# Optimization experiments

Measured on AMD Instinct MI355X. Metric: run time of the kernel, lower is better.

Reference implementation:

```python
import jax, jax.numpy as jnp
import numpy as np

B, N, QD, H, D = 2, 2048, 1152, 16, 72
INNER = H * D
RETAIN_RATE = 0.4  # layer_count in [4, 64] branch
N_KEEP = int(N * RETAIN_RATE)
N_PRUNE = N - N_KEEP
SCALE = D ** (-0.5)


def setup_inputs() -> dict:
    key = jax.random.key(0)
    ks = jax.random.split(key, 6)
    s = 0.02
    return {
        "x": jax.random.normal(ks[0], (B, N, QD), jnp.float32),
        "Wq": jax.random.normal(ks[1], (QD, INNER), jnp.float32) * s,
        "Wk": jax.random.normal(ks[2], (QD, INNER), jnp.float32) * s,
        "Wv": jax.random.normal(ks[3], (QD, INNER), jnp.float32) * s,
        "Wo": jax.random.normal(ks[4], (INNER, QD), jnp.float32) * s,
        "bo": jnp.zeros((QD,), jnp.float32),
    }


def reference(x, Wq, Wk, Wv, Wo, bo):
    b = x.shape[0]
    # self-attention: context = x
    q = (x @ Wq).reshape(b, N, H, D).transpose(0, 2, 1, 3)  # [b,H,N,D]
    k = (x @ Wk).reshape(b, N, H, D).transpose(0, 2, 1, 3)
    v = (x @ Wv).reshape(b, N, H, D).transpose(0, 2, 1, 3)

    # ---- WPR pruning pass: full attention map, mean over heads ----
    logits = jnp.einsum('bhnd,bhmd->bhnm', q, k) * SCALE  # [b,H,N,N]
    M = jax.nn.softmax(logits, axis=-1)
    attn = M.mean(axis=1)  # [b,N,N]

    # 5-step power iteration: dist = (1/N) @ attn^5
    dist = jnp.full((b, 1, N), 1.0 / N, dtype=attn.dtype)
    for _ in range(5):
        dist = dist @ attn
    importance = dist[:, 0]  # [b,N]

    _, imp_inds = jax.lax.top_k(importance, N_KEEP)
    _, prune_inds = jax.lax.top_k(-importance, N_PRUNE)
    # boolean-mask selection in torch returns rows in ascending index order
    sorted_imp = jnp.sort(imp_inds, axis=1)      # [b,N_KEEP]
    sorted_prune = jnp.sort(prune_inds, axis=1)  # [b,N_PRUNE]

    selected_rows = jnp.take_along_axis(attn, sorted_imp[:, :, None], axis=1)  # [b,N_KEEP,N]
    max_inds = jnp.argmax(selected_rows, axis=1)  # [b,N]: most-attending retained row per token
    sim_inds = jnp.take_along_axis(max_inds, sorted_prune, axis=1)  # [b,N_PRUNE]

    # ---- attention among retained tokens only ----
    gi = sorted_imp[:, None, :, None]  # broadcast gather index
    q_r = jnp.take_along_axis(q, gi, axis=2)  # [b,H,N_KEEP,D]
    k_r = jnp.take_along_axis(k, gi, axis=2)
    v_r = jnp.take_along_axis(v, gi, axis=2)
    attn_r = jax.nn.softmax(jnp.einsum('bhnd,bhmd->bhnm', q_r, k_r) * SCALE, axis=-1)
    out_r = jnp.einsum('bhnm,bhmd->bhnd', attn_r, v_r)  # [b,H,N_KEEP,D]
    out_r = out_r.transpose(0, 2, 1, 3).reshape(b, N_KEEP, INNER)

    # similarity-based recovery for pruned tokens
    out_p = jnp.take_along_axis(out_r, sim_inds[:, :, None], axis=1)  # [b,N_PRUNE,INNER]

    bidx = jnp.arange(b)[:, None]
    out = jnp.zeros((b, N, INNER), out_r.dtype)
    out = out.at[bidx, sorted_imp].set(out_r)
    out = out.at[bidx, sorted_prune].set(out_p)

    return out @ Wo + bo
```

## Files before the change

kernel.cpp:

```cpp
#include <hip/hip_runtime.h>

namespace {
constexpr int B = 2;
constexpr int N = 2048;
constexpr int QD = 1152;
constexpr int H = 16;
constexpr int D = 72;
constexpr int INNER = 1152;
constexpr int NKEEP = 819;
constexpr int PSL = 32;
constexpr int ILEN = N / PSL;
constexpr int DP = 80;
constexpr int LSTR = 88;
constexpr int ASL = 16;
constexpr int ACH = (NKEEP + ASL - 1) / ASL;
constexpr int ROWS = B * H * N;
constexpr int X4 = (B * N * QD) / 4;
}

#define FINF __builtin_inff()
#define SCALE 0.11785113019775793f

typedef __attribute__((ext_vector_type(8))) __bf16 bf16x8;
typedef __attribute__((ext_vector_type(16))) float f32x16;
typedef __attribute__((ext_vector_type(8))) short short8;
typedef __attribute__((ext_vector_type(4))) short short4v;

__device__ __forceinline__ f32x16 mfma_bf16(bf16x8 a, bf16x8 b, f32x16 c) {
  return __builtin_amdgcn_mfma_f32_32x32x16_bf16(a, b, c, 0, 0, 0);
}
__device__ __forceinline__ short f2bf(float x) {
  unsigned u = __float_as_uint(x);
  unsigned r = (u + 0x7fffu + ((u >> 16) & 1u)) >> 16;
  return (short)r;
}
__device__ __forceinline__ float bf2f(short b) {
  return __uint_as_float(((unsigned)(unsigned short)b) << 16);
}

__global__ __launch_bounds__(256) void k_prep(
    const float* __restrict__ X, short* __restrict__ Xh, short* __restrict__ Xl,
    short* __restrict__ qkv)
{
  int g = blockIdx.x * 256 + threadIdx.x;
  if (g < X4) {
    float4 v = ((const float4*)X)[g];
    float vv[4] = {v.x, v.y, v.z, v.w};
    short4v h, l;
#pragma unroll
    for (int i = 0; i < 4; ++i) {
      short hb = f2bf(vv[i]);
      h[i] = hb;
      l[i] = f2bf(vv[i] - bf2f(hb));
    }
    *(short4v*)(void*)(Xh + (size_t)g * 4) = h;
    *(short4v*)(void*)(Xl + (size_t)g * 4) = l;
  } else {
    int t = g - X4;
    int arr = t / ROWS, row = t - arr * ROWS;
    *(float4*)(void*)(qkv + (size_t)arr * ROWS * DP + (size_t)row * DP + 72) =
        make_float4(0.f, 0.f, 0.f, 0.f);
  }
}

__global__ __launch_bounds__(256) void k_wsplit4(
    const float* __restrict__ W0, const float* __restrict__ W1,
    const float* __restrict__ W2, const float* __restrict__ W3,
    short* __restrict__ WTh, short* __restrict__ WTl,
    short* __restrict__ WoTh, short* __restrict__ WoTl)
{
  __shared__ float tile[64][65];
  const int tid = threadIdx.x;
  const int k0 = blockIdx.y * 64, n0 = blockIdx.x * 64;
  const int z = blockIdx.z;
  const float* W = (z == 0) ? W0 : (z == 1) ? W1 : (z == 2) ? W2 : W3;
  short* outH = (z < 3) ? WTh + (size_t)z * QD * INNER : WoTh;
  short* outL = (z < 3) ? WTl + (size_t)z * QD * INNER : WoTl;
  {
    int r = tid >> 2, c0 = (tid & 3) * 16;
#pragma unroll
    for (int j = 0; j < 16; j += 4) {
      float4 v = *(const float4*)&W[(size_t)(k0 + r) * 1152 + n0 + c0 + j];
      tile[r][c0 + j] = v.x; tile[r][c0 + j + 1] = v.y;
      tile[r][c0 + j + 2] = v.z; tile[r][c0 + j + 3] = v.w;
    }
  }
  __syncthreads();
  for (int e = tid; e < 4096; e += 256) {
    int nr = e >> 6, kc = e & 63;
    float v = tile[kc][nr];
    short hb = f2bf(v);
    outH[(size_t)(n0 + nr) * 1152 + k0 + kc] = hb;
    outL[(size_t)(n0 + nr) * 1152 + k0 + kc] = f2bf(v - bf2f(hb));
  }
}

__global__ __launch_bounds__(256, 2) void k_pgemm3(
    const short* __restrict__ Ah_g, const short* __restrict__ Al_g,
    const short* __restrict__ Bh_g, const short* __restrict__ Bl_g,
    short* __restrict__ QKV0)
{
  constexpr int LK = 40;
  __shared__ short AhS[128 * LK], AlS[128 * LK], BhS[128 * LK], BlS[128 * LK];
  const int tid = threadIdx.x;
  const int wv = tid >> 6, ln = tid & 63;
  const int col = ln & 31, hi = ln >> 5;
  const int wm = wv >> 1, wn = wv & 1;
  const int swz = (blockIdx.x & 7) * 108 + (blockIdx.x >> 3);
  const int m0 = (swz / 27) * 128, n0 = (swz % 27) * 128;

  f32x16 acc[2][2];
#pragma unroll
  for (int mi = 0; mi < 2; ++mi)
#pragma unroll
    for (int ni = 0; ni < 2; ++ni)
#pragma unroll
      for (int r = 0; r < 16; ++r) acc[mi][ni][r] = 0.f;

  for (int kt = 0; kt < 1152; kt += 32) {
    __syncthreads();
    for (int e = tid; e < 512; e += 256) {
      int r = e >> 2, c4 = e & 3;
      size_t sa = (size_t)(m0 + r) * 1152 + kt + c4 * 8;
      *(float4*)&AhS[r * LK + c4 * 8] = *(const float4*)(Ah_g + sa);
      *(float4*)&AlS[r * LK + c4 * 8] = *(const float4*)(Al_g + sa);
      size_t sb = (size_t)(n0 + r) * 1152 + kt + c4 * 8;
      *(float4*)&BhS[r * LK + c4 * 8] = *(const float4*)(Bh_g + sb);
      *(float4*)&BlS[r * LK + c4 * 8] = *(const float4*)(Bl_g + sb);
    }
    __syncthreads();
#pragma unroll
    for (int kc = 0; kc < 2; ++kc) {
      bf16x8 ah[2], al[2], bh[2], bl[2];
#pragma unroll
      for (int mi = 0; mi < 2; ++mi) {
        int r = wm * 64 + mi * 32 + col;
        ah[mi] = *(const bf16x8*)&AhS[r * LK + kc * 16 + hi * 8];
        al[mi] = *(const bf16x8*)&AlS[r * LK + kc * 16 + hi * 8];
      }
#pragma unroll
      for (int ni = 0; ni < 2; ++ni) {
        int r = wn * 64 + ni * 32 + col;
        bh[ni] = *(const bf16x8*)&BhS[r * LK + kc * 16 + hi * 8];
        bl[ni] = *(const bf16x8*)&BlS[r * LK + kc * 16 + hi * 8];
      }
#pragma unroll
      for (int mi = 0; mi < 2; ++mi)
#pragma unroll
        for (int ni = 0; ni < 2; ++ni) {
          acc[mi][ni] = mfma_bf16(ah[mi], bh[ni], acc[mi][ni]);
          acc[mi][ni] = mfma_bf16(ah[mi], bl[ni], acc[mi][ni]);
          acc[mi][ni] = mfma_bf16(al[mi], bh[ni], acc[mi][ni]);
        }
    }
  }
  const size_t S = (size_t)65536 * 80;
#pragma unroll
  for (int mi = 0; mi < 2; ++mi)
#pragma unroll
    for (int ni = 0; ni < 2; ++ni)
#pragma unroll
      for (int r = 0; r < 16; ++r) {
        int m = m0 + wm * 64 + mi * 32 + (r & 3) + 8 * (r >> 2) + 4 * hi;
        int c = n0 + wn * 64 + ni * 32 + col;
        int which = c / 1152, cm = c - which * 1152;
        int hh = cm / 72, dd = cm - hh * 72;
        int b = m >> 11, nn = m & 2047;
        size_t idx = (((size_t)(b * 16 + hh)) * 2048 + nn) * 80 + dd;
        float v = acc[mi][ni][r];
        short hb = f2bf(v);
        short* OH = QKV0 + (size_t)which * 2 * S;
        OH[idx] = hb;
        OH[S + idx] = f2bf(v - bf2f(hb));
      }
}

__global__ __launch_bounds__(256, 2) void k_stats3(
    const short* __restrict__ Qh, const short* __restrict__ Ql,
    const short* __restrict__ Kh, const short* __restrict__ Kl,
    float* __restrict__ ssum)
{
  __shared__ __align__(16) short kh[64 * LSTR];
  __shared__ __align__(16) short kl[64 * LSTR];
  const int tid = threadIdx.x;
  const int wv = tid >> 6, ln = tid & 63;
  const int col = ln & 31, hi = ln >> 5;
  const int hb = blockIdx.x & 31;
  const int rest = blockIdx.x >> 5;
  const int q0 = (rest & 7) * 256;
  const int ks = rest >> 3;
  const int h = hb >> 1, b = hb & 1;
  const size_t bhbase = (size_t)(b * H + h) * N * DP;
  const int kbeg = ks * (N / 2), kend = kbeg + N / 2;

  bf16x8 qfh[2][5], qfl[2][5];
#pragma unroll
  for (int mi = 0; mi < 2; ++mi) {
    const size_t rb = bhbase + (size_t)(q0 + wv * 64 + mi * 32 + col) * DP + hi * 8;
#pragma unroll
    for (int d = 0; d < 5; ++d) {
      qfh[mi][d] = *(const bf16x8*)(const void*)(Qh + rb + d * 16);
      qfl[mi][d] = *(const bf16x8*)(const void*)(Ql + rb + d * 16);
    }
  }
  float s[2][16];
#pragma unroll
  for (int mi = 0; mi < 2; ++mi)
#pragma unroll
    for (int r = 0; r < 16; ++r) s[mi][r] = 0.f;

  float4 rkh[3], rkl[3];
  auto LOADK = [&](int kt) {
#pragma unroll
    for (int ss = 0; ss < 3; ++ss) {
      int e = ss * 256 + tid;
      if (e < 640) {
        int r = e / 10, cc = e - r * 10;
        size_t sb = bhbase + (size_t)(kt + r) * DP + cc * 8;
        rkh[ss] = *(const float4*)(const void*)(Kh + sb);
        rkl[ss] = *(const float4*)(const void*)(Kl + sb);
      }
    }
  };
  auto STOREK = [&]() {
#pragma unroll
    for (int ss = 0; ss < 3; ++ss) {
      int e = ss * 256 + tid;
      if (e < 640) {
        int r = e / 10, cc = e - r * 10;
        *(float4*)(void*)(kh + r * LSTR + cc * 8) = rkh[ss];
        *(float4*)(void*)(kl + r * LSTR + cc * 8) = rkl[ss];
      }
    }
  };

  LOADK(kbeg);
  for (int kt = kbeg; kt < kend; kt += 64) {
    __syncthreads();
    STOREK();
    __syncthreads();
    if (kt + 64 < kend) LOADK(kt + 64);
    f32x16 z[2][2];
#pragma unroll
    for (int mi = 0; mi < 2; ++mi)
#pragma unroll
      for (int rn = 0; rn < 2; ++rn)
#pragma unroll
        for (int r = 0; r < 16; ++r) z[mi][rn][r] = 0.f;
#pragma unroll
    for (int d = 0; d < 5; ++d) {
      const int boff = d * 16 + hi * 8;
      bf16x8 bh0 = *(const bf16x8*)(const void*)(kh + col * LSTR + boff);
      bf16x8 bl0 = *(const bf16x8*)(const void*)(kl + col * LSTR + boff);
      bf16x8 bh1 = *(const bf16x8*)(const void*)(kh + (32 + col) * LSTR + boff);
      bf16x8 bl1 = *(const bf16x8*)(const void*)(kl + (32 + col) * LSTR + boff);
#pragma unroll
      for (int mi = 0; mi < 2; ++mi) {
        z[mi][0] = mfma_bf16(qfh[mi][d], bh0, z[mi][0]);
        z[mi][0] = mfma_bf16(qfh[mi][d], bl0, z[mi][0]);
        z[mi][0] = mfma_bf16(qfl[mi][d], bh0, z[mi][0]);
        z[mi][1] = mfma_bf16(qfh[mi][d], bh1, z[mi][1]);
        z[mi][1] = mfma_bf16(qfh[mi][d], bl1, z[mi][1]);
        z[mi][1] = mfma_bf16(qfl[mi][d], bh1, z[mi][1]);
      }
    }
#pragma unroll
    for (int mi = 0; mi < 2; ++mi)
#pragma unroll
      for (int r = 0; r < 16; ++r)
        s[mi][r] += __expf(z[mi][0][r] * SCALE) + __expf(z[mi][1][r] * SCALE);
  }
#pragma unroll
  for (int mi = 0; mi < 2; ++mi)
#pragma unroll
    for (int r = 0; r < 16; ++r) {
      float v = s[mi][r];
#pragma unroll
      for (int o = 1; o < 32; o <<= 1) v += __shfl_xor(v, o);
      if (col == 0) {
        int row = q0 + wv * 64 + mi * 32 + ((r & 3) + ((r >> 2) << 3) + (hi << 2));
        ssum[(size_t)ks * ROWS + (size_t)(b * H + h) * N + row] = v;
      }
    }
}

__global__ __launch_bounds__(256) void k_sinv(
    const float* __restrict__ ssum, float* __restrict__ inv_out)
{
  int g = blockIdx.x * 256 + threadIdx.x;
  if (g < ROWS) inv_out[g] = 1.0f / (ssum[g] + ssum[(size_t)ROWS + g]);
}

__global__ __launch_bounds__(256, 2) void k_attn3(
    const short* __restrict__ Qh, const short* __restrict__ Ql,
    const short* __restrict__ Kh, const short* __restrict__ Kl,
    const float* __restrict__ inv_in, float* __restrict__ attn,
    float* __restrict__ part8)
{
  __shared__ __align__(16) short kh[64 * LSTR];
  __shared__ __align__(16) short kl[64 * LSTR];
  __shared__ float invs[256];
  __shared__ float colred[64][8];
  const int tid = threadIdx.x;
  const int wv = tid >> 6, ln = tid & 63;
  const int col = ln & 31, hi = ln >> 5;
  const int q0 = (blockIdx.x & 7) * 256;
  const int b = (blockIdx.x >> 3) & 1;
  const int k0 = (blockIdx.x >> 4) * 64;

  f32x16 pa[2][2];
#pragma unroll
  for (int mi = 0; mi < 2; ++mi)
#pragma unroll
    for (int rn = 0; rn < 2; ++rn)
#pragma unroll
      for (int r = 0; r < 16; ++r) pa[mi][rn][r] = 0.f;

  float4 rkh[3], rkl[3];
  float rin;
  auto LOADH = [&](int h) {
    const size_t hb = (size_t)(b * H + h) * N * DP;
#pragma unroll
    for (int ss = 0; ss < 3; ++ss) {
      int e = ss * 256 + tid;
      if (e < 640) {
        int r = e / 10, cc = e - r * 10;
        size_t sb = hb + (size_t)(k0 + r) * DP + cc * 8;
        rkh[ss] = *(const float4*)(const void*)(Kh + sb);
        rkl[ss] = *(const float4*)(const void*)(Kl + sb);
      }
    }
    rin = inv_in[(size_t)(b * H + h) * N + q0 + tid];
  };
  auto STOREH = [&]() {
#pragma unroll
    for (int ss = 0; ss < 3; ++ss) {
      int e = ss * 256 + tid;
      if (e < 640) {
        int r = e / 10, cc = e - r * 10;
        *(float4*)(void*)(kh + r * LSTR + cc * 8) = rkh[ss];
        *(float4*)(void*)(kl + r * LSTR + cc * 8) = rkl[ss];
      }
    }
    invs[tid] = rin;
  };

  LOADH(0);
  for (int h = 0; h < H; ++h) {
    __syncthreads();
    STOREH();
    __syncthreads();
    if (h + 1 < H) LOADH(h + 1);

    const size_t bhbase = (size_t)(b * H + h) * N * DP;
    f32x16 z[2][2];
#pragma unroll
    for (int mi = 0; mi < 2; ++mi)
#pragma unroll
      for (int rn = 0; rn < 2; ++rn)
#pragma unroll
        for (int r = 0; r < 16; ++r) z[mi][rn][r] = 0.f;

#pragma unroll
    for (int d = 0; d < 5; ++d) {
      const int boff = d * 16 + hi * 8;
      bf16x8 bh0 = *(const bf16x8*)(const void*)(kh + col * LSTR + boff);
      bf16x8 bl0 = *(const bf16x8*)(const void*)(kl + col * LSTR + boff);
      bf16x8 bh1 = *(const bf16x8*)(const void*)(kh + (32 + col) * LSTR + boff);
      bf16x8 bl1 = *(const bf16x8*)(const void*)(kl + (32 + col) * LSTR + boff);
      bf16x8 qh0 = *(const bf16x8*)(const void*)(Qh + bhbase + (size_t)(q0 + wv * 64 + col) * DP + boff);
      bf16x8 ql0 = *(const bf16x8*)(const void*)(Ql + bhbase + (size_t)(q0 + wv * 64 + col) * DP + boff);
      bf16x8 qh1 = *(const bf16x8*)(const void*)(Qh + bhbase + (size_t)(q0 + wv * 64 + 32 + col) * DP + boff);
      bf16x8 ql1 = *(const bf16x8*)(const void*)(Ql + bhbase + (size_t)(q0 + wv * 64 + 32 + col) * DP + boff);
      z[0][0] = mfma_bf16(qh0, bh0, z[0][0]);
      z[0][0] = mfma_bf16(qh0, bl0, z[0][0]);
      z[0][0] = mfma_bf16(ql0, bh0, z[0][0]);
      z[0][1] = mfma_bf16(qh0, bh1, z[0][1]);
      z[0][1] = mfma_bf16(qh0, bl1, z[0][1]);
      z[0][1] = mfma_bf16(ql0, bh1, z[0][1]);
      z[1][0] = mfma_bf16(qh1, bh0, z[1][0]);
      z[1][0] = mfma_bf16(qh1, bl0, z[1][0]);
      z[1][0] = mfma_bf16(ql1, bh0, z[1][0]);
      z[1][1] = mfma_bf16(qh1, bh1, z[1][1]);
      z[1][1] = mfma_bf16(qh1, bl1, z[1][1]);
      z[1][1] = mfma_bf16(ql1, bh1, z[1][1]);
    }
#pragma unroll
    for (int mi = 0; mi < 2; ++mi)
#pragma unroll
      for (int r = 0; r < 16; ++r) {
        const int rloc = wv * 64 + mi * 32 + (r & 3) + ((r >> 2) << 3) + (hi << 2);
        const float iv = invs[rloc];
        pa[mi][0][r] += __expf(z[mi][0][r] * SCALE) * iv;
        pa[mi][1][r] += __expf(z[mi][1][r] * SCALE) * iv;
      }
  }
  const float invH = 1.0f / H;
#pragma unroll
  for (int mi = 0; mi < 2; ++mi)
#pragma unroll
    for (int r = 0; r < 16; ++r) {
      const int row = q0 + wv * 64 + mi * 32 + (r & 3) + ((r >> 2) << 3) + (hi << 2);
      attn[((size_t)b * N + row) * N + k0 + col] = pa[mi][0][r] * invH;
      attn[((size_t)b * N + row) * N + k0 + 32 + col] = pa[mi][1][r] * invH;
    }
  __syncthreads();
#pragma unroll
  for (int rn = 0; rn < 2; ++rn) {
    float s = 0.f;
#pragma unroll
    for (int mi = 0; mi < 2; ++mi)
#pragma unroll
      for (int r = 0; r < 16; ++r) s += pa[mi][rn][r];
    colred[rn * 32 + col][wv * 2 + hi] = s * invH;
  }
  __syncthreads();
  if (tid < 64) {
    float s = 0.f;
#pragma unroll
    for (int u = 0; u < 8; ++u) s += colred[tid][u];
    part8[(size_t)(q0 >> 8) * (B * N) + b * N + k0 + tid] = s * (1.0f / N);
  }
}

__global__ __launch_bounds__(256) void k_powfused(
    const float* __restrict__ attn, const float* __restrict__ partial_in,
    float* __restrict__ partial_out, int nin)
{
  __shared__ float red[4][64];
  __shared__ float ds[64];
  const int tid = threadIdx.x;
  const int g = blockIdx.x * 256 + tid;
  const int sy = blockIdx.y;
  const int b = g / N, j = g % N;
  const int i0 = sy * ILEN;
  {
    int i = tid & 63, sgrp = tid >> 6;
    const int per = nin >> 2;
    const float* p = partial_in + (size_t)(b * N + i0 + i);
    float s8 = 0.f;
    for (int k = 0; k < per; ++k) s8 += p[(size_t)(sgrp * per + k) * (B * N)];
    red[sgrp][i] = s8;
  }
  __syncthreads();
  if (tid < 64) ds[tid] = red[0][tid] + red[1][tid] + red[2][tid] + red[3][tid];
  __syncthreads();
  const float* ab = attn + (size_t)b * N * N;
  float s0 = 0.f, s1 = 0.f, s2 = 0.f, s3 = 0.f;
  for (int i = 0; i < ILEN; i += 4) {
    s0 += ds[i + 0] * ab[(size_t)(i0 + i + 0) * N + j];
    s1 += ds[i + 1] * ab[(size_t)(i0 + i + 1) * N + j];
    s2 += ds[i + 2] * ab[(size_t)(i0 + i + 2) * N + j];
    s3 += ds[i + 3] * ab[(size_t)(i0 + i + 3) * N + j];
  }
  partial_out[(size_t)sy * (B * N) + g] = (s0 + s1) + (s2 + s3);
}

__global__ __launch_bounds__(1024) void k_partition(
    const float* __restrict__ partial, int* __restrict__ sorted_imp,
    int* __restrict__ keepflag, int* __restrict__ s_map)
{
  __shared__ float v[N];
  __shared__ int   id[N];
  __shared__ int   kf[N];
  __shared__ int   ps[N];
  const int tid = threadIdx.x;
  const int b = blockIdx.x;
  for (int i = tid; i < N; i += 1024) {
    float s = 0.f;
    const float* p = partial + (size_t)(b * N + i);
    for (int sy = 0; sy < PSL; ++sy) s += p[(size_t)sy * (B * N)];
    v[i] = s; id[i] = i;
  }
  for (int k = 2; k <= N; k <<= 1) {
    for (int j = k >> 1; j > 0; j >>= 1) {
      __syncthreads();
      for (int i = tid; i < N; i += 1024) {
        int ixj = i ^ j;
        if (ixj > i) {
          bool up = ((i & k) == 0);
          float va = v[i], vb = v[ixj];
          int ia = id[i], ib = id[ixj];
          bool b_before_a = (vb > va) || (vb == va && ib < ia);
          if (b_before_a == up) { v[i] = vb; v[ixj] = va; id[i] = ib; id[ixj] = ia; }
        }
      }
    }
  }
  __syncthreads();
  for (int i = tid; i < N; i += 1024) kf[id[i]] = (i < NKEEP) ? 1 : 0;
  __syncthreads();
  for (int i = tid; i < N; i += 1024) ps[i] = kf[i];
  for (int off = 1; off < N; off <<= 1) {
    __syncthreads();
    int t0 = (tid >= off) ? ps[tid - off] : 0;
    int i1 = tid + 1024;
    int t1 = ps[i1 - off];
    __syncthreads();
    ps[tid] += t0;
    ps[i1] += t1;
  }
  __syncthreads();
  for (int i = tid; i < N; i += 1024) {
    int excl = ps[i] - kf[i];
    keepflag[b * N + i] = kf[i];
    if (kf[i]) { sorted_imp[b * NKEEP + excl] = i; s_map[b * N + i] = excl; }
  }
}

__global__ __launch_bounds__(256) void k_argmax_part(
    const float* __restrict__ attn, const int* __restrict__ sorted_imp,
    float* __restrict__ pval, int* __restrict__ pidx)
{
  __shared__ int imp_s[ACH];
  const int tid = threadIdx.x;
  const int g = blockIdx.x * 256 + tid;
  const int s = blockIdx.y;
  const int b = g / N, n = g % N;
  const int k0 = s * ACH;
  const int k1 = (k0 + ACH < NKEEP) ? k0 + ACH : NKEEP;
  const int cnt = k1 - k0;
  for (int i = tid; i < cnt; i += 256) imp_s[i] = sorted_imp[b * NKEEP + k0 + i];
  __syncthreads();
  const float* ab = attn + (size_t)b * N * N;
  float best = -FINF; int bi = k0;
  for (int k = 0; k < cnt; ++k) {
    float val = ab[(size_t)imp_s[k] * N + n];
    if (val > best) { best = val; bi = k0 + k; }
  }
  pval[(size_t)s * (B * N) + g] = best;
  pidx[(size_t)s * (B * N) + g] = bi;
}

__global__ __launch_bounds__(256) void k_argmax_comb(
    const float* __restrict__ pval, const int* __restrict__ pidx,
    const int* __restrict__ keepflag, int* __restrict__ s_map)
{
  int g = blockIdx.x * 256 + threadIdx.x;
  if (g >= B * N) return;
  float best = -FINF; int bi = 0;
#pragma unroll
  for (int s = 0; s < ASL; ++s) {
    float v = pval[(size_t)s * (B * N) + g];
    if (v > best) { best = v; bi = pidx[(size_t)s * (B * N) + g]; }
  }
  if (!keepflag[g]) s_map[g] = bi;
}

__global__ __launch_bounds__(256, 2) void k_rfused(
    const short* __restrict__ Qh, const short* __restrict__ Ql,
    const short* __restrict__ Kh, const short* __restrict__ Kl,
    const short* __restrict__ Vh, const int* __restrict__ sorted_imp,
    short* __restrict__ Yh, short* __restrict__ Yl)
{
  constexpr int LK = 88;
  constexpr int VTS = 72;
  __shared__ __align__(16) short KhS[64 * LK];
  __shared__ __align__(16) short KlS[64 * LK];
  __shared__ __align__(16) short VhS[64 * LK];
  __shared__ __align__(16) short VT[72 * VTS];
  __shared__ int imp[NKEEP];
  const int tid = threadIdx.x;
  const int wv = tid >> 6, ln = tid & 63;
  const int col = ln & 31, hi = ln >> 5;
  const int b = blockIdx.z, h = blockIdx.y, q0 = blockIdx.x * 128;
  const size_t bh80 = (size_t)(b * H + h) * N * DP;
  for (int i = tid; i < NKEEP; i += 256) imp[i] = sorted_imp[b * NKEEP + i];
  __syncthreads();
  int qr = q0 + wv * 32 + col;
  int qi = imp[qr < NKEEP ? qr : NKEEP - 1];
  bf16x8 qfh[5], qfl[5];
  {
    const size_t qb = bh80 + (size_t)qi * DP + hi * 8;
#pragma unroll
    for (int d = 0; d < 5; ++d) {
      qfh[d] = *(const bf16x8*)(const void*)(Qh + qb + d * 16);
      qfl[d] = *(const bf16x8*)(const void*)(Ql + qb + d * 16);
    }
  }
  float denom = 0.f;
  f32x16 oacc[3];
#pragma unroll
  for (int nc = 0; nc < 3; ++nc)
#pragma unroll
    for (int r = 0; r < 16; ++r) oacc[nc][r] = 0.f;

  for (int kt = 0; kt < 832; kt += 64) {
    for (int e = tid; e < 640; e += 256) {
      int r = e / 10, cc = e - r * 10;
      int kv = kt + r;
      float4 vkh, vkl, vvh;
      if (kv < NKEEP) {
        size_t sb = bh80 + (size_t)imp[kv] * DP + cc * 8;
        vkh = *(const float4*)(const void*)(Kh + sb);
        vkl = *(const float4*)(const void*)(Kl + sb);
        vvh = *(const float4*)(const void*)(Vh + sb);
      } else {
        vkh = make_float4(0.f, 0.f, 0.f, 0.f); vkl = vkh; vvh = vkh;
      }
      *(float4*)(void*)&KhS[r * LK + cc * 8] = vkh;
      *(float4*)(void*)&KlS[r * LK + cc * 8] = vkl;
      *(float4*)(void*)&VhS[r * LK + cc * 8] = vvh;
    }
    __syncthreads();
    f32x16 z[2];
#pragma unroll
    for (int rn = 0; rn < 2; ++rn)
#pragma unroll
      for (int r = 0; r < 16; ++r) z[rn][r] = 0.f;
#pragma unroll
    for (int d = 0; d < 5; ++d) {
      const int boff = d * 16 + hi * 8;
#pragma unroll
      for (int rn = 0; rn < 2; ++rn) {
        bf16x8 kfh = *(const bf16x8*)(const void*)(KhS + (rn * 32 + col) * LK + boff);
        bf16x8 kfl = *(const bf16x8*)(const void*)(KlS + (rn * 32 + col) * LK + boff);
        z[rn] = mfma_bf16(kfh, qfh[d], z[rn]);
        z[rn] = mfma_bf16(kfh, qfl[d], z[rn]);
        z[rn] = mfma_bf16(kfl, qfh[d], z[rn]);
      }
    }
    for (int e = tid; e < 576; e += 256) {
      int dd = e % 72, k8 = e / 72;
      short8 t;
#pragma unroll
      for (int j = 0; j < 8; ++j) t[j] = VhS[(k8 * 8 + j) * LK + dd];
      *(short8*)(void*)&VT[dd * VTS + k8 * 8] = t;
    }
    const bool full = (kt + 64 <= NKEEP);
#pragma unroll
    for (int rn = 0; rn < 2; ++rn) {
      int kvb = kt + rn * 32 + 4 * hi;
#pragma unroll
      for (int r = 0; r < 16; ++r) {
        float pe = __expf(z[rn][r] * SCALE);
        if (!full) {
          int kv = kvb + (r & 3) + 8 * (r >> 2);
          pe = (kv < NKEEP) ? pe : 0.f;
        }
        z[rn][r] = pe;
        denom += pe;
      }
    }
    __syncthreads();
#pragma unroll
    for (int rn = 0; rn < 2; ++rn) {
#pragma unroll
      for (int kc = 0; kc < 2; ++kc) {
        unsigned p0, p1, p2, p3;
        asm("v_cvt_pk_bf16_f32 %0, %1, %2" : "=v"(p0) : "v"(z[rn][8 * kc + 0]), "v"(z[rn][8 * kc + 1]));
        asm("v_cvt_pk_bf16_f32 %0, %1, %2" : "=v"(p1) : "v"(z[rn][8 * kc + 2]), "v"(z[rn][8 * kc + 3]));
        asm("v_cvt_pk_bf16_f32 %0, %1, %2" : "=v"(p2) : "v"(z[rn][8 * kc + 4]), "v"(z[rn][8 * kc + 5]));
        asm("v_cvt_pk_bf16_f32 %0, %1, %2" : "=v"(p3) : "v"(z[rn][8 * kc + 6]), "v"(z[rn][8 * kc + 7]));
        unsigned othA = hi ? p0 : p2, othB = hi ? p1 : p3;
        unsigned swA = (unsigned)__shfl_xor((int)othA, 32);
        unsigned swB = (unsigned)__shfl_xor((int)othB, 32);
        union { unsigned u[4]; bf16x8 v; } pf;
        pf.u[0] = hi ? swA : p0; pf.u[1] = hi ? swB : p1;
        pf.u[2] = hi ? p2 : swA; pf.u[3] = hi ? p3 : swB;
        const int kb = rn * 32 + kc * 16 + hi * 8;
#pragma unroll
        for (int nc = 0; nc < 3; ++nc) {
          int dr = nc * 32 + col; if (dr > 71) dr = 71;
          bf16x8 vf = *(const bf16x8*)(const void*)(VT + dr * VTS + kb);
          oacc[nc] = mfma_bf16(pf.v, vf, oacc[nc]);
        }
      }
    }
  }
  denom += __shfl_xor(denom, 32);
  float invd = 1.0f / denom;
#pragma unroll
  for (int r = 0; r < 16; ++r) {
    int cr = (r & 3) + 8 * (r >> 2) + 4 * hi;
    int q = q0 + wv * 32 + cr;
    float dv = __shfl(invd, cr);
    if (q < NKEEP) {
#pragma unroll
      for (int nc = 0; nc < 3; ++nc) {
        int dd = nc * 32 + col;
        if (dd < 72) {
          float v = oacc[nc][r] * dv;
          size_t idx = ((size_t)b * NKEEP + q) * 1152 + h * 72 + dd;
          short hb = f2bf(v);
          Yh[idx] = hb;
          Yl[idx] = f2bf(v - bf2f(hb));
        }
      }
    }
  }
}

__global__ __launch_bounds__(256, 2) void k_ogemm(
    const short* __restrict__ Ah_g, const short* __restrict__ Al_g,
    const short* __restrict__ Bh_g, const short* __restrict__ Bl_g,
    const int* __restrict__ sorted_imp,
    float* __restrict__ OutF, const float* __restrict__ bias,
    int Mtot)
{
  constexpr int LK = 40;
  __shared__ short AhS[64 * LK], AlS[64 * LK], BhS[64 * LK], BlS[64 * LK];
  const int tid = threadIdx.x;
  const int wv = tid >> 6, ln = tid & 63;
  const int col = ln & 31, hi = ln >> 5;
  const int wm = wv >> 1, wn = wv & 1;
  const int m0 = blockIdx.y * 64, n0 = blockIdx.x * 64;
  f32x16 acc;
#pragma unroll
  for (int r = 0; r < 16; ++r) acc[r] = 0.f;

  for (int kt = 0; kt < 1152; kt += 32) {
    __syncthreads();
    {
      int e = tid;
      int r = e >> 2, c4 = e & 3;
      int ra = m0 + r; if (ra >= Mtot) ra = Mtot - 1;
      size_t sa = (size_t)ra * 1152 + kt + c4 * 8;
      *(float4*)&AhS[r * LK + c4 * 8] = *(const float4*)(Ah_g + sa);
      *(float4*)&AlS[r * LK + c4 * 8] = *(const float4*)(Al_g + sa);
      size_t sb = (size_t)(n0 + r) * 1152 + kt + c4 * 8;
      *(float4*)&BhS[r * LK + c4 * 8] = *(const float4*)(Bh_g + sb);
      *(float4*)&BlS[r * LK + c4 * 8] = *(const float4*)(Bl_g + sb);
    }
    __syncthreads();
#pragma unroll
    for (int kc = 0; kc < 2; ++kc) {
      int ra = wm * 32 + col;
      int rb = wn * 32 + col;
      bf16x8 ah = *(const bf16x8*)&AhS[ra * LK + kc * 16 + hi * 8];
      bf16x8 al = *(const bf16x8*)&AlS[ra * LK + kc * 16 + hi * 8];
      bf16x8 bh = *(const bf16x8*)&BhS[rb * LK + kc * 16 + hi * 8];
      bf16x8 bl = *(const bf16x8*)&BlS[rb * LK + kc * 16 + hi * 8];
      acc = mfma_bf16(ah, bh, acc);
      acc = mfma_bf16(ah, bl, acc);
      acc = mfma_bf16(al, bh, acc);
    }
  }
#pragma unroll
  for (int r = 0; r < 16; ++r) {
    int m = m0 + wm * 32 + (r & 3) + 8 * (r >> 2) + 4 * hi;
    int c = n0 + wn * 32 + col;
    if (m < Mtot) {
      int b = m / NKEEP, mm = m - b * NKEEP;
      int orig = sorted_imp[b * NKEEP + mm];
      OutF[((size_t)b * N + orig) * 1152 + c] = acc[r] + bias[c];
    }
  }
}

__global__ __launch_bounds__(256) void k_prune(
    const int* __restrict__ keepflag, const int* __restrict__ sorted_imp,
    const int* __restrict__ s_map, float* __restrict__ out)
{
  size_t g = (size_t)blockIdx.x * 256 + threadIdx.x;
  if (g >= (size_t)B * N * QD) return;
  int c = (int)(g % QD);
  int n_ = (int)((g / QD) % N);
  int b = (int)(g / ((size_t)N * QD));
  if (keepflag[b * N + n_]) return;
  int src = sorted_imp[b * NKEEP + s_map[b * N + n_]];
  out[g] = out[((size_t)b * N + src) * QD + c];
}

extern "C" void kernel_launch(void* const* d_in, const int* in_sizes, int n_in,
                              void* d_out, int out_size, void* d_ws, size_t ws_size,
                              hipStream_t stream)
{
  const float* x  = (const float*)d_in[0];
  const float* Wq = (const float*)d_in[1];
  const float* Wk = (const float*)d_in[2];
  const float* Wv = (const float*)d_in[3];
  const float* Wo = (const float*)d_in[4];
  const float* bo = (const float*)d_in[5];
  float* out = (float*)d_out;

  char* ws = (char*)d_ws;
  size_t off = 0;
  auto alloc = [&](size_t bytes) -> void* {
    void* p = ws + off;
    off = (off + bytes + 255) & ~(size_t)255;
    return p;
  };
  const size_t XEL = (size_t)B * N * QD;
  const size_t WEL = (size_t)QD * INNER;
  short* xh   = (short*)alloc(sizeof(short) * XEL);
  short* xl   = (short*)alloc(sizeof(short) * XEL);
  short* WTh  = (short*)alloc(sizeof(short) * WEL * 3);
  short* WTl  = (short*)alloc(sizeof(short) * WEL * 3);
  short* WoTh = (short*)alloc(sizeof(short) * WEL);
  short* WoTl = (short*)alloc(sizeof(short) * WEL);
  short* Qhb  = (short*)alloc(sizeof(short) * (size_t)ROWS * DP);
  short* Qlb  = (short*)alloc(sizeof(short) * (size_t)ROWS * DP);
  short* Khb  = (short*)alloc(sizeof(short) * (size_t)ROWS * DP);
  short* Klb  = (short*)alloc(sizeof(short) * (size_t)ROWS * DP);
  short* Vhb  = (short*)alloc(sizeof(short) * (size_t)ROWS * DP);
  short* Vlb  = (short*)alloc(sizeof(short) * (size_t)ROWS * DP);
  float* attn = (float*)alloc(sizeof(float) * (size_t)B * N * N);
  float* ssum = (float*)alloc(sizeof(float) * 2 * (size_t)ROWS);
  float* inv  = (float*)alloc(sizeof(float) * (size_t)ROWS);
  float* partA = (float*)alloc(sizeof(float) * PSL * B * N);
  float* partB = (float*)alloc(sizeof(float) * PSL * B * N);
  int* sorted_imp = (int*)alloc(sizeof(int) * B * NKEEP);
  int* keepflag   = (int*)alloc(sizeof(int) * B * N);
  int* s_map      = (int*)alloc(sizeof(int) * B * N);
  float* pval     = (float*)alloc(sizeof(float) * ASL * B * N);
  int*   pidx     = (int*)alloc(sizeof(int) * ASL * B * N);
  (void)Vlb;
  short* Yh = xh;
  short* Yl = xh + (size_t)B * NKEEP * INNER;

  dim3 blk(256);

  k_prep<<<dim3((X4 + 6 * ROWS) / 256), blk, 0, stream>>>(x, xh, xl, Qhb);
  k_wsplit4<<<dim3(QD / 64, QD / 64, 4), blk, 0, stream>>>(
      Wq, Wk, Wv, Wo, WTh, WTl, WoTh, WoTl);

  k_pgemm3<<<dim3(864), blk, 0, stream>>>(xh, xl, WTh, WTl, Qhb);

  k_stats3<<<dim3(512), blk, 0, stream>>>(Qhb, Qlb, Khb, Klb, ssum);
  k_sinv<<<dim3(ROWS / 256), blk, 0, stream>>>(ssum, inv);
  k_attn3<<<dim3(512), blk, 0, stream>>>(Qhb, Qlb, Khb, Klb, inv, attn, partB);

  k_powfused<<<dim3(B * N / 256, PSL), blk, 0, stream>>>(attn, partB, partA, 8);
  k_powfused<<<dim3(B * N / 256, PSL), blk, 0, stream>>>(attn, partA, partB, 32);
  k_powfused<<<dim3(B * N / 256, PSL), blk, 0, stream>>>(attn, partB, partA, 32);
  k_powfused<<<dim3(B * N / 256, PSL), blk, 0, stream>>>(attn, partA, partB, 32);

  k_partition<<<dim3(B), dim3(1024), 0, stream>>>(partB, sorted_imp, keepflag, s_map);
  k_argmax_part<<<dim3(B * N / 256, ASL), blk, 0, stream>>>(attn, sorted_imp, pval, pidx);
  k_argmax_comb<<<dim3(B * N / 256), blk, 0, stream>>>(pval, pidx, keepflag, s_map);

  k_rfused<<<dim3((NKEEP + 127) / 128, H, B), blk, 0, stream>>>(
      Qhb, Qlb, Khb, Klb, Vhb, sorted_imp, Yh, Yl);

  k_ogemm<<<dim3(QD / 64, (B * NKEEP + 63) / 64), blk, 0, stream>>>(
      Yh, Yl, WoTh, WoTl, sorted_imp, out, bo, B * NKEEP);
  k_prune<<<dim3((int)(((size_t)B * N * QD + 255) / 256)), blk, 0, stream>>>(
      keepflag, sorted_imp, s_map, out);
}
```

Baseline: 503.2 us.

## Split retained-token attention over key range and combine partial outputs

The retained-token attention kernel now splits the key loop into two halves across extra blocks in grid z. This doubles the block count from 224, which is below the 256 CUs, to 448. Each half writes unnormalized fp32 partial outputs (reusing the attn buffer) and partial softmax denominators. A new combine kernel sums them, normalizes, and produces the bf16 hi/lo split. The trade-off is extra global memory traffic and one more launch in exchange for better CU occupancy.

```diff
diff --git a/kernel.cpp b/kernel.cpp
--- a/kernel.cpp
+++ b/kernel.cpp
@@ -16,6 +16,8 @@
 constexpr int ACH = (NKEEP + ASL - 1) / ASL;
 constexpr int ROWS = B * H * N;
 constexpr int X4 = (B * N * QD) / 4;
+constexpr size_t OSZ = (size_t)B * NKEEP * INNER;
+constexpr int DSZ = B * H * NKEEP;
 }
 
 #define FINF __builtin_inff()
@@ -551,7 +553,7 @@
     const short* __restrict__ Qh, const short* __restrict__ Ql,
     const short* __restrict__ Kh, const short* __restrict__ Kl,
     const short* __restrict__ Vh, const int* __restrict__ sorted_imp,
-    short* __restrict__ Yh, short* __restrict__ Yl)
+    float* __restrict__ Opart, float* __restrict__ dpart)
 {
   constexpr int LK = 88;
   constexpr int VTS = 72;
@@ -563,7 +565,9 @@
   const int tid = threadIdx.x;
   const int wv = tid >> 6, ln = tid & 63;
   const int col = ln & 31, hi = ln >> 5;
-  const int b = blockIdx.z, h = blockIdx.y, q0 = blockIdx.x * 128;
+  const int b = blockIdx.z & 1, ks = blockIdx.z >> 1;
+  const int h = blockIdx.y, q0 = blockIdx.x * 128;
+  const int kbeg = ks ? 448 : 0, kend = ks ? 832 : 448;
   const size_t bh80 = (size_t)(b * H + h) * N * DP;
   for (int i = tid; i < NKEEP; i += 256) imp[i] = sorted_imp[b * NKEEP + i];
   __syncthreads();
@@ -585,7 +589,7 @@
 #pragma unroll
     for (int r = 0; r < 16; ++r) oacc[nc][r] = 0.f;
 
-  for (int kt = 0; kt < 832; kt += 64) {
+  for (int kt = kbeg; kt < kend; kt += 64) {
     for (int e = tid; e < 640; e += 256) {
       int r = e / 10, cc = e - r * 10;
       int kv = kt + r;
@@ -668,27 +672,43 @@
       }
     }
   }
-  denom += __shfl_xor(denom, 32);
-  float invd = 1.0f / denom;
 #pragma unroll
   for (int r = 0; r < 16; ++r) {
     int cr = (r & 3) + 8 * (r >> 2) + 4 * hi;
     int q = q0 + wv * 32 + cr;
-    float dv = __shfl(invd, cr);
     if (q < NKEEP) {
 #pragma unroll
       for (int nc = 0; nc < 3; ++nc) {
         int dd = nc * 32 + col;
-        if (dd < 72) {
-          float v = oacc[nc][r] * dv;
-          size_t idx = ((size_t)b * NKEEP + q) * 1152 + h * 72 + dd;
-          short hb = f2bf(v);
-          Yh[idx] = hb;
-          Yl[idx] = f2bf(v - bf2f(hb));
-        }
-      }
-    }
-  }
+        if (dd < 72)
+          Opart[(size_t)ks * OSZ + ((size_t)b * NKEEP + q) * 1152 + h * 72 + dd] =
+              oacc[nc][r];
+      }
+    }
+  }
+  denom += __shfl_xor(denom, 32);
+  if (hi == 0) {
+    int q = q0 + wv * 32 + col;
+    if (q < NKEEP)
+      dpart[ks * DSZ + (b * H + h) * NKEEP + q] = denom;
+  }
+}
+
+__global__ __launch_bounds__(256) void k_rcomb(
+    const float* __restrict__ Opart, const float* __restrict__ dpart,
+    short* __restrict__ Yh, short* __restrict__ Yl)
+{
+  size_t g = (size_t)blockIdx.x * 256 + threadIdx.x;
+  int c = (int)(g % 1152);
+  int q = (int)((g / 1152) % NKEEP);
+  int b = (int)(g / ((size_t)NKEEP * 1152));
+  int h = c / 72;
+  float o = Opart[g] + Opart[OSZ + g];
+  float d = dpart[(b * H + h) * NKEEP + q] + dpart[DSZ + (b * H + h) * NKEEP + q];
+  float v = o * (1.0f / d);
+  short hb = f2bf(v);
+  Yh[g] = hb;
+  Yl[g] = f2bf(v - bf2f(hb));
 }
 
 __global__ __launch_bounds__(256, 2) void k_ogemm(
@@ -800,6 +820,7 @@
   float* inv  = (float*)alloc(sizeof(float) * (size_t)ROWS);
   float* partA = (float*)alloc(sizeof(float) * PSL * B * N);
   float* partB = (float*)alloc(sizeof(float) * PSL * B * N);
+  float* dpart = (float*)alloc(sizeof(float) * 2 * DSZ);
   int* sorted_imp = (int*)alloc(sizeof(int) * B * NKEEP);
   int* keepflag   = (int*)alloc(sizeof(int) * B * N);
   int* s_map      = (int*)alloc(sizeof(int) * B * N);
@@ -808,6 +829,7 @@
   (void)Vlb;
   short* Yh = xh;
   short* Yl = xh + (size_t)B * NKEEP * INNER;
+  float* Opart = attn;
 
   dim3 blk(256);
 
@@ -830,8 +852,9 @@
   k_argmax_part<<<dim3(B * N / 256, ASL), blk, 0, stream>>>(attn, sorted_imp, pval, pidx);
   k_argmax_comb<<<dim3(B * N / 256), blk, 0, stream>>>(pval, pidx, keepflag, s_map);
 
-  k_rfused<<<dim3((NKEEP + 127) / 128, H, B), blk, 0, stream>>>(
-      Qhb, Qlb, Khb, Klb, Vhb, sorted_imp, Yh, Yl);
+  k_rfused<<<dim3((NKEEP + 127) / 128, H, 2 * B), blk, 0, stream>>>(
+      Qhb, Qlb, Khb, Klb, Vhb, sorted_imp, Opart, dpart);
+  k_rcomb<<<dim3((int)(OSZ / 256)), blk, 0, stream>>>(Opart, dpart, Yh, Yl);
 
   k_ogemm<<<dim3(QD / 64, (B * NKEEP + 63) / 64), blk, 0, stream>>>(
       Yh, Yl, WoTh, WoTl, sorted_imp, out, bo, B * NKEEP);
```

Result: no change. 494.0 us (-1.8%).
